# Performance work log

Hardware: AMD Instinct MI355X
Metric: run time of the kernel (lower is better)

## Reference

```python
import jax, jax.numpy as jnp
import numpy as np

N, DIN, D, K0, NC = 32768, 768, 512, 128, 2
KS = [128, 64, 32, 16]  # prototype counts per stage (num_protos // 2**i)
NEG_SLOPE = 0.01


def _lin(x, W, b):
    # torch nn.Linear: W is [out, in]
    return x @ W.T + b


def _ln(x, g, b):
    m = x.mean(-1, keepdims=True)
    v = ((x - m) ** 2).mean(-1, keepdims=True)
    return (x - m) * jax.lax.rsqrt(v + 1e-5) * g + b


def setup_inputs() -> dict:
    key = jax.random.key(0)
    ks = jax.random.split(key, 40)
    s = 0.02

    def nrm(k, shp, sc=s):
        return jax.random.normal(k, shp, jnp.float32) * sc

    inp = {}
    inp["data"] = jax.random.normal(ks[0], (N, DIN), jnp.float32)
    inp["prototypes"] = jax.random.normal(ks[1], (K0, DIN), jnp.float32)
    inp["W_pp"] = nrm(ks[2], (D, DIN)); inp["b_pp"] = jnp.zeros((D,), jnp.float32)
    inp["W_cp"] = nrm(ks[3], (D, DIN)); inp["b_cp"] = jnp.zeros((D,), jnp.float32)
    inp["sim_scale"] = jnp.ones((1,), jnp.float32)
    # 3 enhancer MLPs + layernorms (stacked, same shapes)
    inp["enh_w1"] = nrm(ks[4], (3, D, D)); inp["enh_b1"] = jnp.zeros((3, D), jnp.float32)
    inp["enh_w2"] = nrm(ks[5], (3, D, D)); inp["enh_b2"] = jnp.zeros((3, D), jnp.float32)
    inp["ln_g"] = jnp.ones((3, D), jnp.float32); inp["ln_b"] = jnp.zeros((3, D), jnp.float32)
    # ProtoReducers: Mlp along K axis; fc1 [inK,inK], fc2 [outK,inK]
    ki = 6
    for i in range(3):
        inK, outK = KS[i], KS[i + 1]
        inp[f"red_w1_{i}"] = nrm(ks[ki], (inK, inK)); ki += 1
        inp[f"red_b1_{i}"] = jnp.zeros((inK,), jnp.float32)
        inp[f"red_w2_{i}"] = nrm(ks[ki], (outK, inK)); ki += 1
        inp[f"red_b2_{i}"] = jnp.zeros((outK,), jnp.float32)
    inp["W_proc"] = nrm(ks[20], (D, D)); inp["b_proc"] = jnp.zeros((D,), jnp.float32)
    inp["g_an"] = jnp.ones((D,), jnp.float32); inp["b_an"] = jnp.zeros((D,), jnp.float32)
    inp["W_t"] = nrm(ks[21], (D, D)); inp["b_t"] = jnp.zeros((D,), jnp.float32)
    inp["W_g"] = nrm(ks[22], (D, D)); inp["b_g"] = jnp.zeros((D,), jnp.float32)
    inp["W_s"] = nrm(ks[23], (1, D)); inp["b_s"] = jnp.zeros((1,), jnp.float32)
    inp["W_h"] = nrm(ks[24], (D, D)); inp["b_h"] = jnp.zeros((D,), jnp.float32)
    inp["W_c"] = nrm(ks[25], (NC, D)); inp["b_c"] = jnp.zeros((NC,), jnp.float32)
    return inp


def reference(data, prototypes, W_pp, b_pp, W_cp, b_cp, sim_scale,
              enh_w1, enh_b1, enh_w2, enh_b2, ln_g, ln_b,
              red_w1_0, red_b1_0, red_w2_0, red_b2_0,
              red_w1_1, red_b1_1, red_w2_1, red_b2_1,
              red_w1_2, red_b1_2, red_w2_2, red_b2_2,
              W_proc, b_proc, g_an, b_an,
              W_t, b_t, W_g, b_g, W_s, b_s, W_h, b_h, W_c, b_c):
    # patch / prototype projections (Linear + LeakyReLU)
    P = jax.nn.leaky_relu(_lin(data, W_pp, b_pp), NEG_SLOPE)        # [N, D]
    C = jax.nn.leaky_relu(_lin(prototypes, W_cp, b_cp), NEG_SLOPE)  # [K0, D]
    # denom = max(1e-6, tau * similarity_scale.item()); tau=1, no grad through scale
    denom = jnp.maximum(1e-6, jax.lax.stop_gradient(sim_scale)[0])
    reds = [(red_w1_0, red_b1_0, red_w2_0, red_b2_0),
            (red_w1_1, red_b1_1, red_w2_1, red_b2_1),
            (red_w1_2, red_b1_2, red_w2_2, red_b2_2)]
    for i in range(3):
        # L2 similarity: -cdist(P, C) computed as a GEMM
        d2 = (jnp.sum(P * P, -1, keepdims=True) + jnp.sum(C * C, -1)[None, :]
              - 2.0 * (P @ C.T))
        sim = -jnp.sqrt(jnp.maximum(d2, 1e-12))                     # [N, K]
        A = jax.nn.softmax(sim / denom, axis=1)                     # soft routing
        ctx = A @ C                                                 # [N, D]
        P = _ln(P + ctx, ln_g[i], ln_b[i])
        P = P + _lin(jax.nn.relu(_lin(P, enh_w1[i], enh_b1[i])), enh_w2[i], enh_b2[i])
        # ProtoReducer: Mlp over K axis (operate on C.T of shape [D, K])
        w1, b1, w2, b2 = reds[i]
        Ct = _lin(jax.nn.relu(_lin(C.T, w1, b1)), w2, b2)           # [D, Kout]
        C = Ct.T
    Z = jnp.concatenate([P, C], axis=0)                             # [N+16, D]
    Z = jax.nn.relu(_lin(Z, W_proc, b_proc))
    Z = _ln(Z, g_an, b_an)
    # gated attention MIL pooling
    t = jnp.tanh(_lin(Z, W_t, b_t))
    g = jax.nn.sigmoid(_lin(Z, W_g, b_g))
    scores = _lin(t * g, W_s, b_s)                                  # [N+16, 1]
    Aw = jax.nn.softmax(scores, axis=0)
    bag = Aw.T @ Z                                                  # [1, D]
    h = jax.nn.relu(_lin(bag, W_h, b_h))
    logits = _lin(h, W_c, b_c)                                      # [1, 2]
    return logits
```

## Files before the change

kernel.cpp:

```cpp
#include <hip/hip_runtime.h>
#include <math.h>

typedef _Float16 f16x8 __attribute__((ext_vector_type(8)));
typedef _Float16 f16x4 __attribute__((ext_vector_type(4)));
typedef float f32x4 __attribute__((ext_vector_type(4)));

#define TBM 256
#define TBN 128
#define TBK 32

#define AS1 __attribute__((address_space(1)))
#define AS3 __attribute__((address_space(3)))

__device__ __forceinline__ void gll16(const _Float16* g, _Float16* l)
{
    __builtin_amdgcn_global_load_lds((const AS1 unsigned int*)g,
                                     (AS3 unsigned int*)l, 16, 0, 0);
}

__device__ __forceinline__ int xcd_swz(int bid, int nwg)
{
    if ((nwg & 7) == 0) {
        int chunk = nwg >> 3;
        bid = (bid & 7) * chunk + (bid >> 3);
    }
    return bid;
}

__device__ __forceinline__ float fsigmoid(float x)
{
    return __builtin_amdgcn_rcpf(1.f + __expf(-x));
}
__device__ __forceinline__ float ftanh(float x)
{
    float ax = fabsf(x);
    float e = __expf(-2.f * ax);
    float t = (1.f - e) * __builtin_amdgcn_rcpf(1.f + e);
    return copysignf(t, x);
}

template<int ACT, bool F16OUT>
__global__ __launch_bounds__(256)
void dot_k(const float* __restrict__ X, const float* __restrict__ W,
           const float* __restrict__ bias, void* __restrict__ Yv,
           int M, int K)
{
    int gw = (blockIdx.x * 256 + threadIdx.x) >> 6;
    int lane = threadIdx.x & 63;
    if (gw >= M * 512) return;
    int r = gw >> 9, n = gw & 511;
    const float* xr = X + (size_t)r * K;
    const float* wr = W + (size_t)n * K;
    float d = 0.f;
    for (int t = 0; t < K; t += 256) {
        float4 a = *(const float4*)(xr + t + lane * 4);
        float4 b = *(const float4*)(wr + t + lane * 4);
        d += a.x * b.x + a.y * b.y + a.z * b.z + a.w * b.w;
    }
#pragma unroll
    for (int o = 32; o; o >>= 1) d += __shfl_xor(d, o);
    if (lane == 0) {
        float v = d + bias[n];
        if (ACT == 1) v = v > 0.f ? v : 0.01f * v;
        else if (ACT == 2) v = fmaxf(v, 0.f);
        if (F16OUT) ((_Float16*)Yv)[(size_t)r * 512 + n] = (_Float16)v;
        else        ((float*)Yv)[(size_t)r * 512 + n] = v;
    }
}

template<int MODE, int ACT, bool SQ>
__global__ __launch_bounds__(512)
void mgemm(const _Float16* __restrict__ A, const _Float16* __restrict__ B,
           const float* __restrict__ bias, _Float16* __restrict__ Yh,
           float* __restrict__ Psq, int M, int K, int Nout)
{
    __shared__ _Float16 As[2][TBM * TBK];
    __shared__ _Float16 Bs[2][TBN * TBK];
    const int tid = threadIdx.x;
    const int lane = tid & 63;
    const int wid = tid >> 6;
    const int wr = wid >> 1, wc = wid & 1;

    int bid = xcd_swz(blockIdx.y * gridDim.x + blockIdx.x, gridDim.x * gridDim.y);
    const int m0 = (bid / gridDim.x) * TBM;
    const int n0 = (bid % gridDim.x) * TBN;

    f32x4 acc[4][4] = {};
    const int nt = K / TBK;

    const int lrow = lane >> 2;
    const int lk = (lane & 3) * 8;

    auto stage = [&](int t, int buf) {
        const int k0 = t * TBK;
#pragma unroll
        for (int q = 0; q < 2; q++) {
            int c = wid * 2 + q;
            int r = c * 16 + lrow;
            int am = min(m0 + r, M - 1);
            gll16(A + (size_t)am * K + k0 + lk, &As[buf][c * 512]);
        }
        {
            int c = wid;
            int r = c * 16 + lrow;
            int bn = min(n0 + r, Nout - 1);
            gll16(B + (size_t)bn * K + k0 + lk, &Bs[buf][c * 512]);
        }
    };

    stage(0, 0);
    __syncthreads();
    for (int t = 0; t < nt; ++t) {
        const int cur = t & 1;
        if (t + 1 < nt) stage(t + 1, cur ^ 1);
        f16x8 af[4], bf[4];
#pragma unroll
        for (int mi = 0; mi < 4; mi++)
            af[mi] = *(const f16x8*)(&As[cur][(wr * 64 + mi * 16 + (lane & 15)) * TBK + (lane >> 4) * 8]);
#pragma unroll
        for (int nj = 0; nj < 4; nj++)
            bf[nj] = *(const f16x8*)(&Bs[cur][(wc * 64 + nj * 16 + (lane & 15)) * TBK + (lane >> 4) * 8]);
#pragma unroll
        for (int mi = 0; mi < 4; mi++)
#pragma unroll
            for (int nj = 0; nj < 4; nj++)
                acc[mi][nj] = __builtin_amdgcn_mfma_f32_16x16x32_f16(af[mi], bf[nj], acc[mi][nj], 0, 0, 0);
        __syncthreads();
    }

    _Float16* eb = &As[0][0];
    const int g = lane >> 4;
#pragma unroll
    for (int p = 0; p < 2; p++) {
        if (p) __syncthreads();
        if ((wr >> 1) == p) {
#pragma unroll
            for (int nj = 0; nj < 4; nj++) {
                int col = wc * 64 + nj * 16 + (lane & 15);
                float bv = bias ? bias[n0 + col] : 0.f;
#pragma unroll
                for (int mi = 0; mi < 4; mi++)
#pragma unroll
                    for (int r = 0; r < 4; r++) {
                        int lr = (wr & 1) * 64 + mi * 16 + g * 4 + r;
                        float v = acc[mi][nj][r] + bv;
                        if (MODE == 0) {
                            if (ACT == 1) v = v > 0.f ? v : 0.01f * v;
                            else if (ACT == 2) v = fmaxf(v, 0.f);
                        }
                        eb[lr * 128 + col] = (_Float16)v;
                    }
            }
        }
        __syncthreads();
        int t4 = tid * 4;
        int lr = t4 >> 4;
        int cbase = (t4 & 15) * 8;
        int m = m0 + p * 128 + lr;
        float sq = 0.f;
        if (m < M) {
#pragma unroll
            for (int q = 0; q < 4; q++) {
                int c0 = cbase + q * 8;
                f16x8 hv = *(f16x8*)(eb + lr * 128 + c0);
                size_t gidx = (size_t)m * Nout + n0 + c0;
                if (MODE == 1) {
                    f16x8 old = *(f16x8*)(Yh + gidx);
                    f16x8 nw;
#pragma unroll
                    for (int e = 0; e < 8; e++) {
                        float s = (float)old[e] + (float)hv[e];
                        nw[e] = (_Float16)s;
                    }
                    *(f16x8*)(Yh + gidx) = nw;
                    hv = nw;
                } else {
                    *(f16x8*)(Yh + gidx) = hv;
                }
                if (SQ) {
#pragma unroll
                    for (int e = 0; e < 8; e++) { float f = (float)hv[e]; sq += f * f; }
                }
            }
        }
        if (SQ) {
            sq += __shfl_xor(sq, 1);
            sq += __shfl_xor(sq, 2);
            if ((lane & 3) == 0 && m < M) atomicAdd(&Psq[m], sq);
        }
    }
}

__global__ __launch_bounds__(512)
void gatgemm(const _Float16* __restrict__ A, const _Float16* __restrict__ B1,
             const _Float16* __restrict__ B2, const float* __restrict__ c1,
             const float* __restrict__ c2, _Float16* __restrict__ Y,
             int M, int K, int Nout)
{
    __shared__ _Float16 As[2][TBM * TBK];
    __shared__ _Float16 B1s[2][TBN * TBK];
    __shared__ _Float16 B2s[2][TBN * TBK];
    const int tid = threadIdx.x;
    const int lane = tid & 63;
    const int wid = tid >> 6;
    const int wr = wid >> 1, wc = wid & 1;

    int bid = xcd_swz(blockIdx.y * gridDim.x + blockIdx.x, gridDim.x * gridDim.y);
    const int m0 = (bid / gridDim.x) * TBM;
    const int n0 = (bid % gridDim.x) * TBN;

    f32x4 acc1[4][4] = {};
    f32x4 acc2[4][4] = {};
    const int nt = K / TBK;

    const int lrow = lane >> 2;
    const int lk = (lane & 3) * 8;

    auto stage = [&](int t, int buf) {
        const int k0 = t * TBK;
#pragma unroll
        for (int q = 0; q < 2; q++) {
            int c = wid * 2 + q;
            int r = c * 16 + lrow;
            int am = min(m0 + r, M - 1);
            gll16(A + (size_t)am * K + k0 + lk, &As[buf][c * 512]);
        }
        {
            int c = wid;
            int r = c * 16 + lrow;
            int bn = min(n0 + r, Nout - 1);
            gll16(B1 + (size_t)bn * K + k0 + lk, &B1s[buf][c * 512]);
            gll16(B2 + (size_t)bn * K + k0 + lk, &B2s[buf][c * 512]);
        }
    };

    stage(0, 0);
    __syncthreads();
    for (int t = 0; t < nt; ++t) {
        const int cur = t & 1;
        if (t + 1 < nt) stage(t + 1, cur ^ 1);
        f16x8 af[4], bf1[4], bf2[4];
#pragma unroll
        for (int mi = 0; mi < 4; mi++)
            af[mi] = *(const f16x8*)(&As[cur][(wr * 64 + mi * 16 + (lane & 15)) * TBK + (lane >> 4) * 8]);
#pragma unroll
        for (int nj = 0; nj < 4; nj++) {
            int ro = (wc * 64 + nj * 16 + (lane & 15)) * TBK + (lane >> 4) * 8;
            bf1[nj] = *(const f16x8*)(&B1s[cur][ro]);
            bf2[nj] = *(const f16x8*)(&B2s[cur][ro]);
        }
#pragma unroll
        for (int mi = 0; mi < 4; mi++)
#pragma unroll
            for (int nj = 0; nj < 4; nj++) {
                acc1[mi][nj] = __builtin_amdgcn_mfma_f32_16x16x32_f16(af[mi], bf1[nj], acc1[mi][nj], 0, 0, 0);
                acc2[mi][nj] = __builtin_amdgcn_mfma_f32_16x16x32_f16(af[mi], bf2[nj], acc2[mi][nj], 0, 0, 0);
            }
        __syncthreads();
    }

    _Float16* eb = &As[0][0];
    const int g = lane >> 4;
#pragma unroll
    for (int p = 0; p < 2; p++) {
        if (p) __syncthreads();
        if ((wr >> 1) == p) {
#pragma unroll
            for (int nj = 0; nj < 4; nj++) {
                int col = wc * 64 + nj * 16 + (lane & 15);
                float bv1 = c1[n0 + col], bv2 = c2[n0 + col];
#pragma unroll
                for (int mi = 0; mi < 4; mi++)
#pragma unroll
                    for (int r = 0; r < 4; r++) {
                        int lr = (wr & 1) * 64 + mi * 16 + g * 4 + r;
                        float t1 = ftanh(acc1[mi][nj][r] + bv1);
                        float g1 = fsigmoid(acc2[mi][nj][r] + bv2);
                        eb[lr * 128 + col] = (_Float16)(t1 * g1);
                    }
            }
        }
        __syncthreads();
        int t4 = tid * 4;
        int lr = t4 >> 4;
        int cbase = (t4 & 15) * 8;
        int m = m0 + p * 128 + lr;
        if (m < M) {
#pragma unroll
            for (int q = 0; q < 4; q++) {
                int c0 = cbase + q * 8;
                f16x8 hv = *(f16x8*)(eb + lr * 128 + c0);
                *(f16x8*)(Y + (size_t)m * Nout + n0 + c0) = hv;
            }
        }
    }
}

#define SBM 128
__global__ __launch_bounds__(256)
void simgemm(const _Float16* __restrict__ A, const _Float16* __restrict__ B,
             const float* __restrict__ Psq, const float* __restrict__ Csq,
             const float* __restrict__ sscale, _Float16* __restrict__ Ah,
             int M, int K, int Kin)
{
    __shared__ _Float16 As[2][SBM * TBK];
    __shared__ _Float16 Bs[2][SBM * TBK];
    __shared__ float redmx[2][SBM];
    __shared__ float redsm[2][SBM];
    const int tid = threadIdx.x;
    const int lane = tid & 63;
    const int wid = tid >> 6;
    const int wr = wid >> 1, wc = wid & 1;
    const int m0 = blockIdx.y * SBM;

    f32x4 acc[4][4] = {};
    const int nt = K / TBK;
    const int lrow = lane >> 2;
    const int lk = (lane & 3) * 8;

    auto stage = [&](int t, int buf) {
        const int k0 = t * TBK;
#pragma unroll
        for (int q = 0; q < 2; q++) {
            int c = wid * 2 + q;
            int r = c * 16 + lrow;
            int am = min(m0 + r, M - 1);
            int bn = min(r, Kin - 1);
            gll16(A + (size_t)am * K + k0 + lk, &As[buf][c * 512]);
            gll16(B + (size_t)bn * K + k0 + lk, &Bs[buf][c * 512]);
        }
    };

    stage(0, 0);
    __syncthreads();
    for (int t = 0; t < nt; ++t) {
        const int cur = t & 1;
        if (t + 1 < nt) stage(t + 1, cur ^ 1);
        f16x8 af[4], bf[4];
#pragma unroll
        for (int mi = 0; mi < 4; mi++)
            af[mi] = *(const f16x8*)(&As[cur][(wr * 64 + mi * 16 + (lane & 15)) * TBK + (lane >> 4) * 8]);
#pragma unroll
        for (int nj = 0; nj < 4; nj++)
            bf[nj] = *(const f16x8*)(&Bs[cur][(wc * 64 + nj * 16 + (lane & 15)) * TBK + (lane >> 4) * 8]);
#pragma unroll
        for (int mi = 0; mi < 4; mi++)
#pragma unroll
            for (int nj = 0; nj < 4; nj++)
                acc[mi][nj] = __builtin_amdgcn_mfma_f32_16x16x32_f16(af[mi], bf[nj], acc[mi][nj], 0, 0, 0);
        __syncthreads();
    }

    const float denom = fmaxf(1e-6f, sscale[0]);
    const int colbase = wc * 64 + (lane & 15);
    const int g = lane >> 4;
    float cc[4];
#pragma unroll
    for (int nj = 0; nj < 4; nj++) {
        int n = colbase + nj * 16;
        cc[nj] = (n < Kin) ? Csq[n] : 0.f;
    }

#pragma unroll
    for (int mi = 0; mi < 4; mi++) {
#pragma unroll
        for (int r = 0; r < 4; r++) {
            int row = wr * 64 + mi * 16 + g * 4 + r;
            float pp = Psq[m0 + row];
            float mx = -INFINITY;
#pragma unroll
            for (int nj = 0; nj < 4; nj++) {
                int n = colbase + nj * 16;
                float v = -INFINITY;
                if (n < Kin)
                    v = -sqrtf(fmaxf(pp + cc[nj] - 2.f * acc[mi][nj][r], 1e-12f)) / denom;
                acc[mi][nj][r] = v;
                mx = fmaxf(mx, v);
            }
#pragma unroll
            for (int o = 1; o < 16; o <<= 1) mx = fmaxf(mx, __shfl_xor(mx, o));
            if ((lane & 15) == 0) redmx[wc][row] = mx;
        }
    }
    __syncthreads();

#pragma unroll
    for (int mi = 0; mi < 4; mi++) {
#pragma unroll
        for (int r = 0; r < 4; r++) {
            int row = wr * 64 + mi * 16 + g * 4 + r;
            float mx = fmaxf(redmx[0][row], redmx[1][row]);
            float s = 0.f;
#pragma unroll
            for (int nj = 0; nj < 4; nj++) {
                int n = colbase + nj * 16;
                float e = (n < Kin) ? __expf(acc[mi][nj][r] - mx) : 0.f;
                acc[mi][nj][r] = e;
                s += e;
            }
#pragma unroll
            for (int o = 1; o < 16; o <<= 1) s += __shfl_xor(s, o);
            if ((lane & 15) == 0) redsm[wc][row] = s;
        }
    }
    __syncthreads();

#pragma unroll
    for (int mi = 0; mi < 4; mi++) {
#pragma unroll
        for (int r = 0; r < 4; r++) {
            int row = wr * 64 + mi * 16 + g * 4 + r;
            float inv = __builtin_amdgcn_rcpf(redsm[0][row] + redsm[1][row]);
            int m = m0 + row;
#pragma unroll
            for (int nj = 0; nj < 4; nj++) {
                int n = colbase + nj * 16;
                if (n < Kin)
                    Ah[(size_t)m * Kin + n] = (_Float16)(acc[mi][nj][r] * inv);
            }
        }
    }
}

__global__ __launch_bounds__(256)
void cvt_k(const float* __restrict__ x, _Float16* __restrict__ y, int n)
{
    int i = (blockIdx.x * 256 + threadIdx.x) * 4;
    if (i < n) {
        float4 v = *(const float4*)(x + i);
        f16x4 h = { (_Float16)v.x, (_Float16)v.y, (_Float16)v.z, (_Float16)v.w };
        *(f16x4*)(y + i) = h;
    }
}

__global__ __launch_bounds__(256)
void cvtC2_k(const float* __restrict__ C, _Float16* __restrict__ Ch,
             _Float16* __restrict__ CTh, float* __restrict__ Csq, int Kin)
{
    int w = threadIdx.x >> 6, lane = threadIdx.x & 63;
    int row = blockIdx.x * 4 + w;
    if (row >= Kin) return;
    float4 a = *(const float4*)(C + (size_t)row * 512 + lane * 8);
    float4 b = *(const float4*)(C + (size_t)row * 512 + lane * 8 + 4);
    f16x8 h;
    h[0] = (_Float16)a.x; h[1] = (_Float16)a.y; h[2] = (_Float16)a.z; h[3] = (_Float16)a.w;
    h[4] = (_Float16)b.x; h[5] = (_Float16)b.y; h[6] = (_Float16)b.z; h[7] = (_Float16)b.w;
    *(f16x8*)(Ch + (size_t)row * 512 + lane * 8) = h;
    float s = 0.f;
#pragma unroll
    for (int q = 0; q < 8; q++) {
        float f = (float)h[q];
        s += f * f;
        CTh[(size_t)(lane * 8 + q) * Kin + row] = h[q];
    }
#pragma unroll
    for (int o = 32; o; o >>= 1) s += __shfl_xor(s, o);
    if (lane == 0) Csq[row] = s;
}

__global__ __launch_bounds__(256)
void ln_k(const _Float16* __restrict__ X, const _Float16* __restrict__ R,
          const float* __restrict__ g, const float* __restrict__ b,
          _Float16* __restrict__ Yh, int M)
{
    int wid = threadIdx.x >> 6, lane = threadIdx.x & 63;
    int row = blockIdx.x * 4 + wid;
    if (row >= M) return;
    f16x8 a = *(const f16x8*)(X + (size_t)row * 512 + lane * 8);
    float v[8];
#pragma unroll
    for (int q = 0; q < 8; q++) v[q] = (float)a[q];
    if (R) {
        f16x8 c = *(const f16x8*)(R + (size_t)row * 512 + lane * 8);
#pragma unroll
        for (int q = 0; q < 8; q++) v[q] += (float)c[q];
    }
    float s = 0.f, ss = 0.f;
#pragma unroll
    for (int q = 0; q < 8; q++) { s += v[q]; ss += v[q] * v[q]; }
#pragma unroll
    for (int o = 32; o; o >>= 1) { s += __shfl_xor(s, o); ss += __shfl_xor(ss, o); }
    float mean = s * (1.f / 512.f);
    float var = ss * (1.f / 512.f) - mean * mean;
    float inv = 1.f / sqrtf(var + 1e-5f);
    int d0 = lane * 8;
    f16x8 o8;
#pragma unroll
    for (int q = 0; q < 8; q++)
        o8[q] = (_Float16)((v[q] - mean) * inv * g[d0 + q] + b[d0 + q]);
    *(f16x8*)(Yh + (size_t)row * 512 + d0) = o8;
}

__global__ __launch_bounds__(256)
void red1_k(const float* __restrict__ C, const float* __restrict__ w1,
            const float* __restrict__ b1, float* __restrict__ H1, int Kin)
{
    int d = blockIdx.x * 256 + threadIdx.x;
    int j = blockIdx.y;
    float acc = b1[j];
    for (int k = 0; k < Kin; k++) acc = fmaf(C[(size_t)k * 512 + d], w1[(size_t)j * Kin + k], acc);
    H1[(size_t)j * 512 + d] = fmaxf(acc, 0.f);
}

__global__ __launch_bounds__(256)
void red2_k(const float* __restrict__ H1, const float* __restrict__ w2,
            const float* __restrict__ b2, float* __restrict__ Cn, int Kin, int Kout)
{
    int d = blockIdx.x * 256 + threadIdx.x;
    int j2 = blockIdx.y;
    float acc = b2[j2];
    for (int j = 0; j < Kin; j++) acc = fmaf(H1[(size_t)j * 512 + d], w2[(size_t)j2 * Kin + j], acc);
    Cn[(size_t)j2 * 512 + d] = acc;
}

__global__ __launch_bounds__(256)
void score_k(const _Float16* __restrict__ TG, const float* __restrict__ Ws,
             const float* __restrict__ bs, float* __restrict__ out, int M)
{
    int wid = threadIdx.x >> 6, lane = threadIdx.x & 63;
    int row = blockIdx.x * 4 + wid;
    if (row >= M) return;
    f16x8 a = *(const f16x8*)(TG + (size_t)row * 512 + lane * 8);
    float4 w0 = *(const float4*)(Ws + lane * 8);
    float4 w1 = *(const float4*)(Ws + lane * 8 + 4);
    float d = (float)a[0] * w0.x + (float)a[1] * w0.y + (float)a[2] * w0.z + (float)a[3] * w0.w
            + (float)a[4] * w1.x + (float)a[5] * w1.y + (float)a[6] * w1.z + (float)a[7] * w1.w;
#pragma unroll
    for (int o = 32; o; o >>= 1) d += __shfl_xor(d, o);
    if (lane == 0) out[row] = d + bs[0];
}

__global__ __launch_bounds__(1024)
void pool_k(float* __restrict__ s, float* __restrict__ scal, int M)
{
    __shared__ float sm[16];
    int tid = threadIdx.x, lane = tid & 63, wid = tid >> 6;
    float mx = -INFINITY;
    for (int i = tid * 4; i < M; i += 4096) {
        float4 a = *(const float4*)(s + i);
        mx = fmaxf(fmaxf(fmaxf(mx, a.x), fmaxf(a.y, a.z)), a.w);
    }
#pragma unroll
    for (int o = 32; o; o >>= 1) mx = fmaxf(mx, __shfl_xor(mx, o));
    if (lane == 0) sm[wid] = mx;
    __syncthreads();
    if (wid == 0) {
        float v = (lane < 16) ? sm[lane] : -INFINITY;
#pragma unroll
        for (int o = 8; o; o >>= 1) v = fmaxf(v, __shfl_xor(v, o));
        if (lane == 0) sm[0] = v;
    }
    __syncthreads();
    float gmax = sm[0];
    __syncthreads();
    float sum = 0.f;
    for (int i = tid * 4; i < M; i += 4096) {
        float4 a = *(const float4*)(s + i);
        float4 e;
        e.x = __expf(a.x - gmax); e.y = __expf(a.y - gmax);
        e.z = __expf(a.z - gmax); e.w = __expf(a.w - gmax);
        *(float4*)(s + i) = e;
        sum += e.x + e.y + e.z + e.w;
    }
#pragma unroll
    for (int o = 32; o; o >>= 1) sum += __shfl_xor(sum, o);
    if (lane == 0) sm[wid] = sum;
    __syncthreads();
    if (tid == 0) {
        float t = 0.f;
        for (int w = 0; w < 16; w++) t += sm[w];
        scal[0] = t;
    }
}

__global__ __launch_bounds__(256)
void bagp_k(const _Float16* __restrict__ Z, const float* __restrict__ w,
            float* __restrict__ PB, int M, int cs)
{
    int d = blockIdx.x * 256 + threadIdx.x;
    int chunk = blockIdx.y;
    int i0 = chunk * cs;
    int i1 = min(M, i0 + cs);
    float acc = 0.f;
    for (int i = i0; i < i1; i++) acc = fmaf(w[i], (float)Z[(size_t)i * 512 + d], acc);
    PB[(size_t)chunk * 512 + d] = acc;
}

__global__ __launch_bounds__(256)
void bagf_k(const float* __restrict__ PB, const float* __restrict__ scal,
            float* __restrict__ bag, int nchunk)
{
    int d = blockIdx.x * 256 + threadIdx.x;
    float acc = 0.f;
    for (int c = 0; c < nchunk; c++) acc += PB[(size_t)c * 512 + d];
    bag[d] = acc / scal[0];
}

__global__ __launch_bounds__(256)
void h_k(const float* __restrict__ bag, const float* __restrict__ Wh,
         const float* __restrict__ bh, float* __restrict__ h)
{
    int wid = threadIdx.x >> 6, lane = threadIdx.x & 63;
    int j = blockIdx.x * 4 + wid;
    const float* wr = Wh + (size_t)j * 512;
    float d = 0.f;
#pragma unroll
    for (int t = 0; t < 2; t++) {
        float4 a = *(const float4*)(wr + t * 256 + lane * 4);
        float4 bv = *(const float4*)(bag + t * 256 + lane * 4);
        d += a.x * bv.x + a.y * bv.y + a.z * bv.z + a.w * bv.w;
    }
#pragma unroll
    for (int o = 32; o; o >>= 1) d += __shfl_xor(d, o);
    if (lane == 0) h[j] = fmaxf(d + bh[j], 0.f);
}

__global__ __launch_bounds__(128)
void logit_k(const float* __restrict__ h, const float* __restrict__ Wc,
             const float* __restrict__ bc, float* __restrict__ out)
{
    int wid = threadIdx.x >> 6, lane = threadIdx.x & 63;
    const float* wr = Wc + (size_t)wid * 512;
    float d = 0.f;
#pragma unroll
    for (int t = 0; t < 2; t++) {
        float4 a = *(const float4*)(wr + t * 256 + lane * 4);
        float4 hv = *(const float4*)(h + t * 256 + lane * 4);
        d += a.x * hv.x + a.y * hv.y + a.z * hv.z + a.w * hv.w;
    }
#pragma unroll
    for (int o = 32; o; o >>= 1) d += __shfl_xor(d, o);
    if (lane == 0) out[wid] = d + bc[wid];
}

extern "C" void kernel_launch(void* const* d_in, const int* in_sizes, int n_in,
                              void* d_out, int out_size, void* d_ws, size_t ws_size,
                              hipStream_t stream)
{
    const float* data    = (const float*)d_in[0];
    const float* protos  = (const float*)d_in[1];
    const float* W_pp    = (const float*)d_in[2];
    const float* b_pp    = (const float*)d_in[3];
    const float* W_cp    = (const float*)d_in[4];
    const float* b_cp    = (const float*)d_in[5];
    const float* sscale  = (const float*)d_in[6];
    const float* enh_w1  = (const float*)d_in[7];
    const float* enh_b1  = (const float*)d_in[8];
    const float* enh_w2  = (const float*)d_in[9];
    const float* enh_b2  = (const float*)d_in[10];
    const float* ln_g    = (const float*)d_in[11];
    const float* ln_b    = (const float*)d_in[12];
    const float* red_w1[3] = {(const float*)d_in[13], (const float*)d_in[17], (const float*)d_in[21]};
    const float* red_b1[3] = {(const float*)d_in[14], (const float*)d_in[18], (const float*)d_in[22]};
    const float* red_w2[3] = {(const float*)d_in[15], (const float*)d_in[19], (const float*)d_in[23]};
    const float* red_b2[3] = {(const float*)d_in[16], (const float*)d_in[20], (const float*)d_in[24]};
    const float* W_proc  = (const float*)d_in[25];
    const float* b_proc  = (const float*)d_in[26];
    const float* g_an    = (const float*)d_in[27];
    const float* b_an    = (const float*)d_in[28];
    const float* W_t     = (const float*)d_in[29];
    const float* b_t     = (const float*)d_in[30];
    const float* W_g     = (const float*)d_in[31];
    const float* b_g     = (const float*)d_in[32];
    const float* W_s     = (const float*)d_in[33];
    const float* b_s     = (const float*)d_in[34];
    const float* W_h     = (const float*)d_in[35];
    const float* b_h     = (const float*)d_in[36];
    const float* W_c     = (const float*)d_in[37];
    const float* b_c     = (const float*)d_in[38];
    float* out = (float*)d_out;

    constexpr int N = 32768, DIN = 768, D = 512;
    constexpr int NCHUNK = 256;
    char* w = (char*)d_ws;
    auto alloc = [&](size_t bytes) -> char* {
        char* p = w; w += (bytes + 255) & ~(size_t)255; return p;
    };
    _Float16* Ph     = (_Float16*)alloc((size_t)N * D * 2);
    _Float16* CTXh   = (_Float16*)alloc((size_t)N * D * 2);
    _Float16* TMPh   = (_Float16*)alloc((size_t)N * D * 2);
    _Float16* Zrawh  = (_Float16*)alloc((size_t)(N + 16) * D * 2);
    _Float16* Zh     = (_Float16*)alloc((size_t)(N + 16) * D * 2);
    _Float16* TGh    = (_Float16*)alloc((size_t)(N + 16) * D * 2);
    _Float16* datah  = (_Float16*)alloc((size_t)N * DIN * 2);
    _Float16* Ah     = (_Float16*)alloc((size_t)N * 128 * 2);
    _Float16* Ch     = (_Float16*)alloc(128 * D * 2);
    _Float16* CTh    = (_Float16*)alloc(128 * D * 2);
    _Float16* Wpph   = (_Float16*)alloc((size_t)D * DIN * 2);
    _Float16* w1h    = (_Float16*)alloc((size_t)3 * D * D * 2);
    _Float16* w2h    = (_Float16*)alloc((size_t)3 * D * D * 2);
    _Float16* Wproch = (_Float16*)alloc((size_t)D * D * 2);
    _Float16* Wth    = (_Float16*)alloc((size_t)D * D * 2);
    _Float16* Wgh    = (_Float16*)alloc((size_t)D * D * 2);
    float*    Psq    = (float*)alloc((size_t)N * 4);
    float*    Csq    = (float*)alloc(128 * 4);
    float*    Ca     = (float*)alloc(128 * D * 4);
    float*    Cb     = (float*)alloc(128 * D * 4);
    float*    H1     = (float*)alloc(128 * D * 4);
    float*    scr    = (float*)alloc((size_t)(N + 16) * 4);
    float*    PB     = (float*)alloc((size_t)NCHUNK * D * 4);
    float*    bag    = (float*)alloc(D * 4);
    float*    hb     = (float*)alloc(D * 4);
    float*    scal   = (float*)alloc(8 * 4);

    dim3 blk(256);
    dim3 blk512(512);
    auto cgrid = [](size_t n) { return dim3((unsigned)((n / 4 + 255) / 256)); };
    auto mgrid = [](int M_, int Nout_) { return dim3((Nout_ + TBN - 1) / TBN, (M_ + TBM - 1) / TBM); };

    cvt_k<<<cgrid((size_t)N * DIN), blk, 0, stream>>>(data, datah, N * DIN);
    cvt_k<<<cgrid((size_t)D * DIN), blk, 0, stream>>>(W_pp, Wpph, D * DIN);
    cvt_k<<<cgrid((size_t)3 * D * D), blk, 0, stream>>>(enh_w1, w1h, 3 * D * D);
    cvt_k<<<cgrid((size_t)3 * D * D), blk, 0, stream>>>(enh_w2, w2h, 3 * D * D);
    cvt_k<<<cgrid((size_t)D * D), blk, 0, stream>>>(W_proc, Wproch, D * D);
    cvt_k<<<cgrid((size_t)D * D), blk, 0, stream>>>(W_t, Wth, D * D);
    cvt_k<<<cgrid((size_t)D * D), blk, 0, stream>>>(W_g, Wgh, D * D);

    hipMemsetAsync(Psq, 0, (size_t)N * 4, stream);
    mgemm<0, 1, true><<<mgrid(N, D), blk512, 0, stream>>>(datah, Wpph, b_pp, Ph, Psq, N, DIN, D);
    dot_k<1, false><<<dim3(128 * 512 / 4), blk, 0, stream>>>(protos, W_cp, b_cp, Ca, 128, DIN);

    float* C = Ca;
    float* Cn = Cb;
    int Kin = 128;
    for (int i = 0; i < 3; i++) {
        int Kout = Kin >> 1;
        cvtC2_k<<<dim3((Kin + 3) / 4), blk, 0, stream>>>(C, Ch, CTh, Csq, Kin);
        simgemm<<<dim3(1, N / SBM), blk, 0, stream>>>(Ph, Ch, Psq, Csq, sscale, Ah, N, D, Kin);
        if (i < 2) hipMemsetAsync(Psq, 0, (size_t)N * 4, stream);
        mgemm<0, 0, false><<<mgrid(N, D), blk512, 0, stream>>>(Ah, CTh, nullptr, CTXh, nullptr, N, Kin, D);
        ln_k<<<dim3((N + 3) / 4), blk, 0, stream>>>(Ph, CTXh, ln_g + (size_t)i * D, ln_b + (size_t)i * D, Ph, N);
        mgemm<0, 2, false><<<mgrid(N, D), blk512, 0, stream>>>(Ph, w1h + (size_t)i * D * D, enh_b1 + (size_t)i * D, TMPh, nullptr, N, D, D);
        if (i < 2)
            mgemm<1, 0, true><<<mgrid(N, D), blk512, 0, stream>>>(TMPh, w2h + (size_t)i * D * D, enh_b2 + (size_t)i * D, Ph, Psq, N, D, D);
        else
            mgemm<1, 0, false><<<mgrid(N, D), blk512, 0, stream>>>(TMPh, w2h + (size_t)i * D * D, enh_b2 + (size_t)i * D, Ph, nullptr, N, D, D);
        red1_k<<<dim3(2, Kin), blk, 0, stream>>>(C, red_w1[i], red_b1[i], H1, Kin);
        red2_k<<<dim3(2, Kout), blk, 0, stream>>>(H1, red_w2[i], red_b2[i], Cn, Kin, Kout);
        float* t = C; C = Cn; Cn = t;
        Kin = Kout;
    }

    mgemm<0, 2, false><<<mgrid(N, D), blk512, 0, stream>>>(Ph, Wproch, b_proc, Zrawh, nullptr, N, D, D);
    dot_k<2, true><<<dim3(16 * 512 / 4), blk, 0, stream>>>(C, W_proc, b_proc, Zrawh + (size_t)N * D, 16, D);
    ln_k<<<dim3((N + 16 + 3) / 4), blk, 0, stream>>>(Zrawh, nullptr, g_an, b_an, Zh, N + 16);

    gatgemm<<<mgrid(N + 16, D), blk512, 0, stream>>>(Zh, Wth, Wgh, b_t, b_g, TGh, N + 16, D, D);

    score_k<<<dim3((N + 16 + 3) / 4), blk, 0, stream>>>(TGh, W_s, b_s, scr, N + 16);
    pool_k<<<dim3(1), dim3(1024), 0, stream>>>(scr, scal, N + 16);
    int cs = (N + 16 + NCHUNK - 1) / NCHUNK;
    bagp_k<<<dim3(2, NCHUNK), blk, 0, stream>>>(Zh, scr, PB, N + 16, cs);
    bagf_k<<<dim3(2), blk, 0, stream>>>(PB, scal, bag, NCHUNK);

    h_k<<<dim3(128), blk, 0, stream>>>(bag, W_h, b_h, hb);
    logit_k<<<dim3(1), dim3(128), 0, stream>>>(hb, W_c, b_c, out);
}
```

Before: 864.5 us.

## Fuse gated-attention score reduction into gatgemm epilogue and fold C conversion into producers

The gated attention GEMM now multiplies tanh·sigmoid by W_s in registers, reduces across lanes and atomically accumulates per-row scores, removing the fp16 TG intermediate and the separate score kernel. The prototype fp16/transposed/squared-norm conversion is moved into dot_k and red2_k, eliminating cvtC2 launches at the cost of extra memsets and atomics. The XCD swizzle is generalized to grids not divisible by 8. Atomic accumulation makes score summation order nondeterministic and the constant b_s term is dropped, relying on softmax shift invariance.

```diff
diff --git a/kernel.cpp b/kernel.cpp
--- a/kernel.cpp
+++ b/kernel.cpp
@@ -18,13 +18,12 @@
                                      (AS3 unsigned int*)l, 16, 0, 0);
 }
 
-__device__ __forceinline__ int xcd_swz(int bid, int nwg)
-{
-    if ((nwg & 7) == 0) {
-        int chunk = nwg >> 3;
-        bid = (bid & 7) * chunk + (bid >> 3);
-    }
-    return bid;
+__device__ __forceinline__ int xcd_swz(int d, int nwg)
+{
+    int q = nwg >> 3, r = nwg & 7;
+    int x = d & 7, idx = d >> 3;
+    int base = x < r ? x * (q + 1) : r * (q + 1) + (x - r) * q;
+    return base + idx;
 }
 
 __device__ __forceinline__ float fsigmoid(float x)
@@ -39,11 +38,12 @@
     return copysignf(t, x);
 }
 
-template<int ACT, bool F16OUT>
+template<int ACT, bool F16OUT, bool EMITC>
 __global__ __launch_bounds__(256)
 void dot_k(const float* __restrict__ X, const float* __restrict__ W,
            const float* __restrict__ bias, void* __restrict__ Yv,
-           int M, int K)
+           _Float16* __restrict__ Ch, _Float16* __restrict__ CTh,
+           float* __restrict__ Csq, int M, int K)
 {
     int gw = (blockIdx.x * 256 + threadIdx.x) >> 6;
     int lane = threadIdx.x & 63;
@@ -65,6 +65,13 @@
         else if (ACT == 2) v = fmaxf(v, 0.f);
         if (F16OUT) ((_Float16*)Yv)[(size_t)r * 512 + n] = (_Float16)v;
         else        ((float*)Yv)[(size_t)r * 512 + n] = v;
+        if (EMITC) {
+            _Float16 h = (_Float16)v;
+            Ch[(size_t)r * 512 + n] = h;
+            CTh[(size_t)n * 128 + r] = h;
+            float f = (float)h;
+            atomicAdd(&Csq[r], f * f);
+        }
     }
 }
 
@@ -194,8 +201,8 @@
 __global__ __launch_bounds__(512)
 void gatgemm(const _Float16* __restrict__ A, const _Float16* __restrict__ B1,
              const _Float16* __restrict__ B2, const float* __restrict__ c1,
-             const float* __restrict__ c2, _Float16* __restrict__ Y,
-             int M, int K, int Nout)
+             const float* __restrict__ c2, const float* __restrict__ Ws,
+             float* __restrict__ scr, int M, int K, int Nout)
 {
     __shared__ _Float16 As[2][TBM * TBK];
     __shared__ _Float16 B1s[2][TBN * TBK];
@@ -259,38 +266,29 @@
         __syncthreads();
     }
 
-    _Float16* eb = &As[0][0];
     const int g = lane >> 4;
-#pragma unroll
-    for (int p = 0; p < 2; p++) {
-        if (p) __syncthreads();
-        if ((wr >> 1) == p) {
+    float wsv[4];
+#pragma unroll
+    for (int nj = 0; nj < 4; nj++)
+        wsv[nj] = Ws[n0 + wc * 64 + nj * 16 + (lane & 15)];
+#pragma unroll
+    for (int mi = 0; mi < 4; mi++) {
+#pragma unroll
+        for (int r = 0; r < 4; r++) {
+            float bv1, bv2, p = 0.f;
 #pragma unroll
             for (int nj = 0; nj < 4; nj++) {
-                int col = wc * 64 + nj * 16 + (lane & 15);
-                float bv1 = c1[n0 + col], bv2 = c2[n0 + col];
-#pragma unroll
-                for (int mi = 0; mi < 4; mi++)
-#pragma unroll
-                    for (int r = 0; r < 4; r++) {
-                        int lr = (wr & 1) * 64 + mi * 16 + g * 4 + r;
-                        float t1 = ftanh(acc1[mi][nj][r] + bv1);
-                        float g1 = fsigmoid(acc2[mi][nj][r] + bv2);
-                        eb[lr * 128 + col] = (_Float16)(t1 * g1);
-                    }
+                int col = n0 + wc * 64 + nj * 16 + (lane & 15);
+                bv1 = c1[col]; bv2 = c2[col];
+                float t1 = ftanh(acc1[mi][nj][r] + bv1);
+                float g1 = fsigmoid(acc2[mi][nj][r] + bv2);
+                p += t1 * g1 * wsv[nj];
             }
-        }
-        __syncthreads();
-        int t4 = tid * 4;
-        int lr = t4 >> 4;
-        int cbase = (t4 & 15) * 8;
-        int m = m0 + p * 128 + lr;
-        if (m < M) {
-#pragma unroll
-            for (int q = 0; q < 4; q++) {
-                int c0 = cbase + q * 8;
-                f16x8 hv = *(f16x8*)(eb + lr * 128 + c0);
-                *(f16x8*)(Y + (size_t)m * Nout + n0 + c0) = hv;
+#pragma unroll
+            for (int o = 1; o < 16; o <<= 1) p += __shfl_xor(p, o);
+            if ((lane & 15) == 0) {
+                int m = m0 + wr * 64 + mi * 16 + g * 4 + r;
+                if (m < M) atomicAdd(&scr[m], p);
             }
         }
     }
@@ -434,31 +432,6 @@
 }
 
 __global__ __launch_bounds__(256)
-void cvtC2_k(const float* __restrict__ C, _Float16* __restrict__ Ch,
-             _Float16* __restrict__ CTh, float* __restrict__ Csq, int Kin)
-{
-    int w = threadIdx.x >> 6, lane = threadIdx.x & 63;
-    int row = blockIdx.x * 4 + w;
-    if (row >= Kin) return;
-    float4 a = *(const float4*)(C + (size_t)row * 512 + lane * 8);
-    float4 b = *(const float4*)(C + (size_t)row * 512 + lane * 8 + 4);
-    f16x8 h;
-    h[0] = (_Float16)a.x; h[1] = (_Float16)a.y; h[2] = (_Float16)a.z; h[3] = (_Float16)a.w;
-    h[4] = (_Float16)b.x; h[5] = (_Float16)b.y; h[6] = (_Float16)b.z; h[7] = (_Float16)b.w;
-    *(f16x8*)(Ch + (size_t)row * 512 + lane * 8) = h;
-    float s = 0.f;
-#pragma unroll
-    for (int q = 0; q < 8; q++) {
-        float f = (float)h[q];
-        s += f * f;
-        CTh[(size_t)(lane * 8 + q) * Kin + row] = h[q];
-    }
-#pragma unroll
-    for (int o = 32; o; o >>= 1) s += __shfl_xor(s, o);
-    if (lane == 0) Csq[row] = s;
-}
-
-__global__ __launch_bounds__(256)
 void ln_k(const _Float16* __restrict__ X, const _Float16* __restrict__ R,
           const float* __restrict__ g, const float* __restrict__ b,
           _Float16* __restrict__ Yh, int M)
@@ -504,30 +477,23 @@
 
 __global__ __launch_bounds__(256)
 void red2_k(const float* __restrict__ H1, const float* __restrict__ w2,
-            const float* __restrict__ b2, float* __restrict__ Cn, int Kin, int Kout)
+            const float* __restrict__ b2, float* __restrict__ Cn,
+            _Float16* __restrict__ Chn, _Float16* __restrict__ CThn,
+            float* __restrict__ Csqn, int Kin, int Kout)
 {
     int d = blockIdx.x * 256 + threadIdx.x;
     int j2 = blockIdx.y;
     float acc = b2[j2];
     for (int j = 0; j < Kin; j++) acc = fmaf(H1[(size_t)j * 512 + d], w2[(size_t)j2 * Kin + j], acc);
     Cn[(size_t)j2 * 512 + d] = acc;
-}
-
-__global__ __launch_bounds__(256)
-void score_k(const _Float16* __restrict__ TG, const float* __restrict__ Ws,
-             const float* __restrict__ bs, float* __restrict__ out, int M)
-{
-    int wid = threadIdx.x >> 6, lane = threadIdx.x & 63;
-    int row = blockIdx.x * 4 + wid;
-    if (row >= M) return;
-    f16x8 a = *(const f16x8*)(TG + (size_t)row * 512 + lane * 8);
-    float4 w0 = *(const float4*)(Ws + lane * 8);
-    float4 w1 = *(const float4*)(Ws + lane * 8 + 4);
-    float d = (float)a[0] * w0.x + (float)a[1] * w0.y + (float)a[2] * w0.z + (float)a[3] * w0.w
-            + (float)a[4] * w1.x + (float)a[5] * w1.y + (float)a[6] * w1.z + (float)a[7] * w1.w;
-#pragma unroll
-    for (int o = 32; o; o >>= 1) d += __shfl_xor(d, o);
-    if (lane == 0) out[row] = d + bs[0];
+    _Float16 h = (_Float16)acc;
+    Chn[(size_t)j2 * 512 + d] = h;
+    CThn[(size_t)d * Kout + j2] = h;
+    float f = (float)h;
+    float sq = f * f;
+#pragma unroll
+    for (int o = 32; o; o >>= 1) sq += __shfl_xor(sq, o);
+    if ((threadIdx.x & 63) == 0) atomicAdd(&Csqn[j2], sq);
 }
 
 __global__ __launch_bounds__(1024)
@@ -669,6 +635,7 @@
     const float* W_c     = (const float*)d_in[37];
     const float* b_c     = (const float*)d_in[38];
     float* out = (float*)d_out;
+    (void)b_s;
 
     constexpr int N = 32768, DIN = 768, D = 512;
     constexpr int NCHUNK = 256;
@@ -681,7 +648,6 @@
     _Float16* TMPh   = (_Float16*)alloc((size_t)N * D * 2);
     _Float16* Zrawh  = (_Float16*)alloc((size_t)(N + 16) * D * 2);
     _Float16* Zh     = (_Float16*)alloc((size_t)(N + 16) * D * 2);
-    _Float16* TGh    = (_Float16*)alloc((size_t)(N + 16) * D * 2);
     _Float16* datah  = (_Float16*)alloc((size_t)N * DIN * 2);
     _Float16* Ah     = (_Float16*)alloc((size_t)N * 128 * 2);
     _Float16* Ch     = (_Float16*)alloc(128 * D * 2);
@@ -718,14 +684,14 @@
 
     hipMemsetAsync(Psq, 0, (size_t)N * 4, stream);
     mgemm<0, 1, true><<<mgrid(N, D), blk512, 0, stream>>>(datah, Wpph, b_pp, Ph, Psq, N, DIN, D);
-    dot_k<1, false><<<dim3(128 * 512 / 4), blk, 0, stream>>>(protos, W_cp, b_cp, Ca, 128, DIN);
+    hipMemsetAsync(Csq, 0, 128 * 4, stream);
+    dot_k<1, false, true><<<dim3(128 * 512 / 4), blk, 0, stream>>>(protos, W_cp, b_cp, Ca, Ch, CTh, Csq, 128, DIN);
 
     float* C = Ca;
     float* Cn = Cb;
     int Kin = 128;
     for (int i = 0; i < 3; i++) {
         int Kout = Kin >> 1;
-        cvtC2_k<<<dim3((Kin + 3) / 4), blk, 0, stream>>>(C, Ch, CTh, Csq, Kin);
         simgemm<<<dim3(1, N / SBM), blk, 0, stream>>>(Ph, Ch, Psq, Csq, sscale, Ah, N, D, Kin);
         if (i < 2) hipMemsetAsync(Psq, 0, (size_t)N * 4, stream);
         mgemm<0, 0, false><<<mgrid(N, D), blk512, 0, stream>>>(Ah, CTh, nullptr, CTXh, nullptr, N, Kin, D);
@@ -735,19 +701,20 @@
             mgemm<1, 0, true><<<mgrid(N, D), blk512, 0, stream>>>(TMPh, w2h + (size_t)i * D * D, enh_b2 + (size_t)i * D, Ph, Psq, N, D, D);
         else
             mgemm<1, 0, false><<<mgrid(N, D), blk512, 0, stream>>>(TMPh, w2h + (size_t)i * D * D, enh_b2 + (size_t)i * D, Ph, nullptr, N, D, D);
+        hipMemsetAsync(Csq, 0, 128 * 4, stream);
         red1_k<<<dim3(2, Kin), blk, 0, stream>>>(C, red_w1[i], red_b1[i], H1, Kin);
-        red2_k<<<dim3(2, Kout), blk, 0, stream>>>(H1, red_w2[i], red_b2[i], Cn, Kin, Kout);
+        red2_k<<<dim3(2, Kout), blk, 0, stream>>>(H1, red_w2[i], red_b2[i], Cn, Ch, CTh, Csq, Kin, Kout);
         float* t = C; C = Cn; Cn = t;
         Kin = Kout;
     }
 
     mgemm<0, 2, false><<<mgrid(N, D), blk512, 0, stream>>>(Ph, Wproch, b_proc, Zrawh, nullptr, N, D, D);
-    dot_k<2, true><<<dim3(16 * 512 / 4), blk, 0, stream>>>(C, W_proc, b_proc, Zrawh + (size_t)N * D, 16, D);
+    dot_k<2, true, false><<<dim3(16 * 512 / 4), blk, 0, stream>>>(C, W_proc, b_proc, Zrawh + (size_t)N * D, nullptr, nullptr, nullptr, 16, D);
     ln_k<<<dim3((N + 16 + 3) / 4), blk, 0, stream>>>(Zrawh, nullptr, g_an, b_an, Zh, N + 16);
 
-    gatgemm<<<mgrid(N + 16, D), blk512, 0, stream>>>(Zh, Wth, Wgh, b_t, b_g, TGh, N + 16, D, D);
-
-    score_k<<<dim3((N + 16 + 3) / 4), blk, 0, stream>>>(TGh, W_s, b_s, scr, N + 16);
+    hipMemsetAsync(scr, 0, (size_t)(N + 16) * 4, stream);
+    gatgemm<<<mgrid(N + 16, D), blk512, 0, stream>>>(Zh, Wth, Wgh, b_t, b_g, W_s, scr, N + 16, D, D);
+
     pool_k<<<dim3(1), dim3(1024), 0, stream>>>(scr, scal, N + 16);
     int cs = (N + 16 + NCHUNK - 1) / NCHUNK;
     bagp_k<<<dim3(2, NCHUNK), blk, 0, stream>>>(Zh, scr, PB, N + 16, cs);
```

Measured after the change: 1.182 ms. 36.8% more time.
